# Performance work log

Measured on AMD Instinct MI355X. Metric: run time of the kernel, lower is better.

## Reference

```python
import jax, jax.numpy as jnp
import numpy as np

B, T, D = 32, 256, 512
P, V = 2048, 40000
DFF = 2148
K_CONCEPT = 50
K_PHENO = 10
EPS = 1e-6


def setup_inputs() -> dict:
    key = jax.random.key(0)
    ks = jax.random.split(key, 10)
    return {
        "visit_embeddings": jax.random.normal(ks[0], (B, T, D), jnp.float32) * 0.05,
        "visit_mask": jax.random.randint(ks[1], (B, T), 0, 2, jnp.int32),
        "embedding_matrix": jax.random.normal(ks[2], (V, D), jnp.float32) * 0.05,
        "phenotype_embeddings": jax.random.normal(ks[3], (P, D), jnp.float32) * 0.05,
        "w1": jax.random.normal(ks[4], (D, DFF), jnp.float32) * (1.0 / np.sqrt(D)),
        "b1": jnp.zeros((DFF,), jnp.float32),
        "w2": jax.random.normal(ks[5], (DFF, D), jnp.float32) * (1.0 / np.sqrt(DFF)),
        "b2": jnp.zeros((D,), jnp.float32),
        "ln1_g": jnp.ones((D,), jnp.float32),
        "ln1_b": jnp.zeros((D,), jnp.float32),
        "ln2_g": jnp.ones((D,), jnp.float32),
        "ln2_b": jnp.zeros((D,), jnp.float32),
    }


def _layer_norm(x, g, b):
    mu = jnp.mean(x, axis=-1, keepdims=True)
    var = jnp.mean(jnp.square(x - mu), axis=-1, keepdims=True)
    return (x - mu) * jax.lax.rsqrt(var + EPS) * g + b


def _smallest_k(x, k):
    # top_k of -x selects the k smallest values per row
    return -jax.lax.top_k(-x, k)[0]


def reference(visit_embeddings, visit_mask, embedding_matrix, phenotype_embeddings,
              w1, b1, w2, b2, ln1_g, ln1_b, ln2_g, ln2_b):
    # mask: original mask==1 means padded; converted mask is 1.0 for valid positions
    conv_mask = (1.0 - visit_mask.astype(jnp.float32))[:, :, None]  # [B,T,1]

    # phenotype attention: softmax over (logits * mask)  (faithful to TF code)
    logits = jnp.einsum('btd,pd->btp', visit_embeddings, phenotype_embeddings) * conv_mask
    probs = jax.nn.softmax(logits, axis=-1)  # [B,T,P]

    # phenotype-concept euclidean distance metric (cdist + row-wise smallest-k)
    r_p = jnp.sum(phenotype_embeddings * phenotype_embeddings, axis=1)[:, None]  # [P,1]
    r_c = jnp.sum(embedding_matrix * embedding_matrix, axis=1)[None, :]          # [1,V]
    d_pc = jnp.sqrt(r_p + r_c - 2.0 * phenotype_embeddings @ embedding_matrix.T)  # [P,V]
    phenotype_concept_dist = jnp.mean(_smallest_k(d_pc, K_CONCEPT))

    # phenotype probability entropy metric
    entropy = -jnp.sum(probs * jnp.log(probs) * conv_mask, axis=-1)  # [B,T]

    # phenotype-phenotype squared-distance metrics
    d_pp = r_p - 2.0 * phenotype_embeddings @ phenotype_embeddings.T + r_p.T  # [P,P]
    near = _smallest_k(d_pp, K_PHENO)  # [P,K_PHENO]
    phe_inv_loss = jnp.mean(jnp.exp(-near))
    phe_dist_metric = jnp.mean(near)
    phe_dist_var = jnp.var(near)

    # residual + FFN block (dropout is identity at inference)
    ctx = probs @ phenotype_embeddings  # [B,T,D]
    out1 = _layer_norm(visit_embeddings + ctx, ln1_g, ln1_b)
    ffn = jnp.maximum(out1 @ w1 + b1, 0.0) @ w2 + b2
    out2 = _layer_norm(out1 + ffn, ln2_g, ln2_b)

    return (out2, probs, phenotype_concept_dist, entropy,
            phe_inv_loss, phe_dist_metric, phe_dist_var)
```

## Files before the change

kernel.cpp:

```cpp
#include <hip/hip_runtime.h>
#include <stdint.h>
#include <stddef.h>

#define BATCH 32
#define TLEN 256
#define DIM 512
#define PHE 2048
#define VOC 40000
#define VOCP 40960
#define DFF 2148
#define DFFP2 2304
#define BT 8192
#define KC 50
#define KP 10
#define CHUNK 8192
#define NCHUNK 5
#define LNEPS 1e-6f
#define BIGF 1e30f

typedef unsigned short u16;
typedef __attribute__((ext_vector_type(8))) short short8;
typedef __attribute__((ext_vector_type(8))) unsigned short ushort8;
typedef __attribute__((ext_vector_type(4))) float floatx4;

__device__ inline u16 f2bf(float f) {
  union { float f; unsigned int u; } v; v.f = f;
  unsigned int u = v.u;
  return (u16)((u + 0x7fffu + ((u >> 16) & 1u)) >> 16);
}
__device__ inline float bf2f(u16 u) {
  union { unsigned int u; float f; } c; c.u = ((unsigned int)u) << 16;
  return c.f;
}

__device__ inline unsigned int f2mono(float f) {
  union { float f; unsigned int u; } c; c.f = f;
  return (c.u & 0x80000000u) ? ~c.u : (c.u | 0x80000000u);
}
__device__ inline float mono2f(unsigned int u) {
  union { unsigned int u; float f; } c;
  c.u = (u & 0x80000000u) ? (u & 0x7FFFFFFFu) : ~u;
  return c.f;
}
__device__ inline unsigned int mono16(u16 u) {
  return (u & 0x8000u) ? (u16)~u : (u16)(u | 0x8000u);
}
__device__ inline float mono2f16(unsigned int k) {
  unsigned int ub = (k & 0x8000u) ? (k & 0x7FFFu) : ((~k) & 0xFFFFu);
  union { unsigned int u; float f; } c; c.u = ub << 16;
  return c.f;
}

__device__ inline void load_lds16(const void* g, void* l) {
  __builtin_amdgcn_global_load_lds(
      (const __attribute__((address_space(1))) unsigned int*)g,
      (__attribute__((address_space(3))) unsigned int*)l, 16, 0, 0);
}

__device__ inline float waveRedSum(float v) {
  #pragma unroll
  for (int off = 32; off > 0; off >>= 1) v += __shfl_down(v, off);
  return v;
}
__device__ inline float waveRedMax(float v) {
  #pragma unroll
  for (int off = 32; off > 0; off >>= 1) v = fmaxf(v, __shfl_down(v, off));
  return v;
}
__device__ inline float blockRedSum(float v) {
  __shared__ float sm[8];
  int lane = threadIdx.x & 63, w = threadIdx.x >> 6, nw = blockDim.x >> 6;
  v = waveRedSum(v);
  __syncthreads();
  if (lane == 0) sm[w] = v;
  __syncthreads();
  float r = 0.f;
  for (int i = 0; i < nw; ++i) r += sm[i];
  return r;
}
__device__ inline float blockRedMax(float v) {
  __shared__ float sm2[8];
  int lane = threadIdx.x & 63, w = threadIdx.x >> 6, nw = blockDim.x >> 6;
  v = waveRedMax(v);
  __syncthreads();
  if (lane == 0) sm2[w] = v;
  __syncthreads();
  float r = -BIGF;
  for (int i = 0; i < nw; ++i) r = fmaxf(r, sm2[i]);
  return r;
}
__device__ inline double blockRedSumD(double v) {
  __shared__ double red[256];
  int tid = threadIdx.x;
  __syncthreads();
  red[tid] = v;
  __syncthreads();
  for (int s = 128; s > 0; s >>= 1) {
    if (tid < s) red[tid] += red[tid + s];
    __syncthreads();
  }
  return red[0];
}

__device__ inline void hist_add2(int* hist, int digit, bool pred) {
  int lane = threadIdx.x & 63;
  unsigned long long act = __ballot(pred);
  if (!act) return;
  int src = __ffsll((long long)act) - 1;
  int ld = __shfl(digit, src);
  unsigned long long m = __ballot(pred && digit == ld);
  if (__popcll(m) >= 32) {
    if (lane == src) atomicAdd(&hist[ld], (int)__popcll(m));
    if ((act & ~m) & (1ull << lane)) atomicAdd(&hist[digit], 1);
  } else {
    if (pred) atomicAdd(&hist[digit], 1);
  }
}

__global__ void k_sentinel(float* out) { out[0] = -12345.0f; }

#define PREP_VIS 2048
#define PREP_PHT (DIM * PHE / 256)
#define PREP_W1  (DFFP2 * DIM / 256)
#define PREP_W2  (DIM * DFFP2 / 256)
__global__ void __launch_bounds__(256) k_prep(
    const float* __restrict__ emb, u16* __restrict__ emb_bf, float* __restrict__ r_c,
    const float* __restrict__ phe, u16* __restrict__ phe_bf, float* __restrict__ r_p,
    const float* __restrict__ visit, u16* __restrict__ visit_bf,
    u16* __restrict__ pheT_bf,
    const float* __restrict__ w1, u16* __restrict__ w1T_bf,
    const float* __restrict__ w2, u16* __restrict__ w2T_bf)
{
  int bid = (int)blockIdx.x, tid = threadIdx.x;
  if (bid < VOC + PHE) {
    const float* src = (bid < VOC) ? emb + (size_t)bid * DIM
                                   : phe + (size_t)(bid - VOC) * DIM;
    u16* dst = (bid < VOC) ? emb_bf + (size_t)bid * DIM
                           : phe_bf + (size_t)(bid - VOC) * DIM;
    float a = src[tid], b = src[tid + 256];
    dst[tid] = f2bf(a); dst[tid + 256] = f2bf(b);
    float s = blockRedSum(a * a + b * b);
    if (tid == 0) {
      if (bid < VOC) r_c[bid] = s; else r_p[bid - VOC] = s;
    }
    return;
  }
  int b2 = bid - (VOC + PHE);
  if (b2 < PREP_VIS) {
    int base = b2 * 2048 + tid;
    #pragma unroll
    for (int e = 0; e < 8; ++e) {
      int i = base + e * 256;
      visit_bf[i] = f2bf(visit[i]);
    }
    return;
  }
  b2 -= PREP_VIS;
  if (b2 < PREP_PHT) {
    int i = b2 * 256 + tid;
    int r = i / PHE, c = i % PHE;
    pheT_bf[i] = f2bf(phe[(size_t)c * DIM + r]);
    return;
  }
  b2 -= PREP_PHT;
  if (b2 < PREP_W1) {
    int i = b2 * 256 + tid;
    int r = i / DIM, c = i % DIM;
    float v = (r < DFF) ? w1[(size_t)c * DFF + r] : 0.f;
    w1T_bf[i] = f2bf(v);
    return;
  }
  b2 -= PREP_W1;
  {
    int i = b2 * 256 + tid;
    int r = i / DFFP2, c = i % DFFP2;
    float v = (c < DFF) ? w2[(size_t)c * DIM + r] : 0.f;
    w2T_bf[i] = f2bf(v);
    return;
  }
}

#define EPI_STORE 0
#define EPI_DPP   1
#define EPI_FFN1  3
#define EPI_FFN2  4

__device__ inline void xcd_block(int BM, int BN, int& m0, int& n0) {
  int nwg = gridDim.x * gridDim.y;
  int orig = blockIdx.y * gridDim.x + blockIdx.x;
  int q = nwg >> 3, r = nwg & 7;
  int xcd = orig & 7, i0 = orig >> 3;
  int wgid = (xcd < r ? xcd * (q + 1) : r * (q + 1) + (xcd - r) * q) + i0;
  m0 = (wgid / gridDim.x) * BM;
  n0 = (wgid % gridDim.x) * BN;
}

template<int EPI>
__device__ inline void epi_write(int rr, int col, float c,
    float* outF, u16* outU, int ldc, const float* rp,
    const float* bias, int nepi) {
  if (EPI == EPI_STORE) {
    outF[(size_t)rr * ldc + col] = c;
  } else if (EPI == EPI_DPP) {
    outF[(size_t)rr * ldc + col] = rp[rr] + rp[col] - 2.f * c;
  } else if (EPI == EPI_FFN1) {
    float h = (col < nepi) ? fmaxf(c + bias[col], 0.f) : 0.f;
    outU[(size_t)rr * ldc + col] = f2bf(h);
  } else if (EPI == EPI_FFN2) {
    outF[(size_t)rr * ldc + col] = c + bias[col];
  }
}

__device__ __forceinline__ void dpc_select(
    char* smem, int si, const u16* __restrict__ dr, int schunk,
    float* __restrict__ top)
{
  int row = si >> 1, half = si & 1;
  const u16* src = dr + (size_t)row * CHUNK + half * 4096;
  int* hist = (int*)smem;
  int* cum  = hist + 1024;
  int* wred = cum + 256;
  int* selb = wred + 8;
  int tid = threadIdx.x, lane = tid & 63, w4 = tid >> 6;
  int hbase = w4 << 8;

  unsigned int kv[16];
  #pragma unroll
  for (int j2 = 0; j2 < 2; ++j2) {
    ushort8 qv = *(const ushort8*)(src + j2 * 2048 + tid * 8);
    #pragma unroll
    for (int e = 0; e < 8; ++e) kv[j2 * 8 + e] = mono16((u16)qv[e]);
  }

  int hbmin = 255, hbmax = 0;
  #pragma unroll
  for (int j = 0; j < 16; ++j) {
    int hb = (int)(kv[j] >> 8);
    hbmin = min(hbmin, hb); hbmax = max(hbmax, hb);
  }
  #pragma unroll
  for (int off = 32; off > 0; off >>= 1) {
    hbmin = min(hbmin, __shfl_down(hbmin, off));
    hbmax = max(hbmax, __shfl_down(hbmax, off));
  }
  if (lane == 0) { wred[w4] = hbmin; wred[4 + w4] = hbmax; }
  __syncthreads();
  int bmin = min(min(wred[0], wred[1]), min(wred[2], wred[3]));
  int bmax = max(max(wred[4], wred[5]), max(wred[6], wred[7]));
  __syncthreads();

  unsigned int prefix;
  int kk = KC;
  if (bmin == bmax) {
    prefix = (unsigned int)bmin;
  } else {
    hist[tid] = 0; hist[tid + 256] = 0; hist[tid + 512] = 0; hist[tid + 768] = 0;
    __syncthreads();
    #pragma unroll
    for (int j = 0; j < 16; ++j) hist_add2(hist + hbase, (int)(kv[j] >> 8), true);
    __syncthreads();
    int x = hist[tid] + hist[tid + 256] + hist[tid + 512] + hist[tid + 768];
    #pragma unroll
    for (int off = 1; off < 64; off <<= 1) { int y = __shfl_up(x, off); if (lane >= off) x += y; }
    if (lane == 63) wred[w4] = x;
    __syncthreads();
    #pragma unroll
    for (int i = 0; i < 4; ++i) if (i < w4) x += wred[i];
    cum[tid] = x;
    __syncthreads();
    int prev = (tid == 0) ? 0 : cum[tid - 1];
    if (prev < kk && kk <= cum[tid]) { selb[0] = tid; selb[1] = kk - prev; }
    __syncthreads();
    prefix = (unsigned int)selb[0];
    kk = selb[1];
    __syncthreads();
  }

  hist[tid] = 0; hist[tid + 256] = 0; hist[tid + 512] = 0; hist[tid + 768] = 0;
  __syncthreads();
  #pragma unroll
  for (int j = 0; j < 16; ++j)
    hist_add2(hist + hbase, (int)(kv[j] & 255u), (kv[j] >> 8) == prefix);
  __syncthreads();
  int x = hist[tid] + hist[tid + 256] + hist[tid + 512] + hist[tid + 768];
  #pragma unroll
  for (int off = 1; off < 64; off <<= 1) { int y = __shfl_up(x, off); if (lane >= off) x += y; }
  if (lane == 63) wred[w4] = x;
  __syncthreads();
  #pragma unroll
  for (int i = 0; i < 4; ++i) if (i < w4) x += wred[i];
  cum[tid] = x;
  __syncthreads();
  int prev = (tid == 0) ? 0 : cum[tid - 1];
  if (prev < kk && kk <= cum[tid]) { selb[0] = tid; selb[1] = kk - prev; }
  __syncthreads();
  unsigned int key = (prefix << 8) | (unsigned int)selb[0];
  float thr = mono2f16(key);
  float* o50 = top + (size_t)row * (NCHUNK * 2 * KC) + (schunk * 2 + half) * KC;
  __syncthreads();

  int cless = 0;
  #pragma unroll
  for (int j = 0; j < 16; ++j) if (kv[j] < key) cless++;
  int xc = cless;
  #pragma unroll
  for (int off = 1; off < 64; off <<= 1) { int y = __shfl_up(xc, off); if (lane >= off) xc += y; }
  if (lane == 63) wred[w4] = xc;
  __syncthreads();
  #pragma unroll
  for (int i = 0; i < 4; ++i) if (i < w4) xc += wred[i];
  int o = xc - cless;
  #pragma unroll
  for (int j = 0; j < 16; ++j)
    if (kv[j] < key) o50[o++] = mono2f16(kv[j]);
  cum[tid] = xc;
  __syncthreads();
  int total_less = cum[255];
  for (int i = total_less + tid; i < KC; i += 256) o50[i] = thr;
}

__global__ void __launch_bounds__(256, 2) k_dpc(
    const u16* __restrict__ phe_bf, const u16* __restrict__ emb_bf,
    int gchunk, int ngemm, u16* __restrict__ dw,
    const u16* __restrict__ dr, int schunk, float* __restrict__ top,
    const float* __restrict__ rp, const float* __restrict__ rc)
{
  __shared__ __align__(16) char smem[32768];
  int bid = (int)blockIdx.x;
  if (bid < ngemm) {
    u16* As = (u16*)smem;
    u16* Bs = (u16*)(smem + 16384);
    int tid = threadIdx.x, lane = tid & 63, w = tid >> 6;
    int wm = w >> 1, wn = w & 1;
    int nwg = ngemm, orig = bid;
    int q = nwg >> 3, r = nwg & 7;
    int xcd = orig & 7, i0 = orig >> 3;
    int wgid = (xcd < r ? xcd * (q + 1) : r * (q + 1) + (xcd - r) * q) + i0;
    int m0 = (wgid >> 6) << 7;
    int n0 = (wgid & 63) << 7;
    const u16* Bm = emb_bf + (size_t)gchunk * CHUNK * DIM;
    const float* rcc = rc + gchunk * CHUNK;
    int bvalid = VOC - gchunk * CHUNK; if (bvalid > CHUNK) bvalid = CHUNK;

    floatx4 acc[4][4];
    #pragma unroll
    for (int i = 0; i < 4; ++i)
      #pragma unroll
      for (int j = 0; j < 4; ++j)
        acc[i][j] = (floatx4){0.f, 0.f, 0.f, 0.f};

    int hi = lane >> 4, rsw = lane & 7;
    for (int kt = 0; kt < DIM / 64; ++kt) {
      int k0 = kt * 64;
      #pragma unroll
      for (int p = 0; p < 4; ++p) {
        int c = p * 256 + tid;
        int row = c >> 3;
        int src16 = (c & 7) ^ (row & 7);
        load_lds16(phe_bf + (size_t)(m0 + row) * DIM + k0 + src16 * 8,
                   &As[p * 2048 + w * 512]);
      }
      #pragma unroll
      for (int p = 0; p < 4; ++p) {
        int c = p * 256 + tid;
        int row = c >> 3;
        int src16 = (c & 7) ^ (row & 7);
        load_lds16(Bm + (size_t)(n0 + row) * DIM + k0 + src16 * 8,
                   &Bs[p * 2048 + w * 512]);
      }
      __syncthreads();
      #pragma unroll
      for (int ks = 0; ks < 2; ++ks) {
        int chk = ((ks << 2) | hi) ^ rsw;
        short8 a[4], b[4];
        #pragma unroll
        for (int i = 0; i < 4; ++i)
          a[i] = *(const short8*)&As[(wm * 64 + i * 16 + (lane & 15)) * 64 + chk * 8];
        #pragma unroll
        for (int j = 0; j < 4; ++j)
          b[j] = *(const short8*)&Bs[(wn * 64 + j * 16 + (lane & 15)) * 64 + chk * 8];
        #pragma unroll
        for (int i = 0; i < 4; ++i)
          #pragma unroll
          for (int j = 0; j < 4; ++j)
            acc[i][j] = __builtin_amdgcn_mfma_f32_16x16x32_bf16(a[i], b[j], acc[i][j], 0, 0, 0);
      }
      __syncthreads();
    }
    #pragma unroll
    for (int i = 0; i < 4; ++i) {
      #pragma unroll
      for (int j = 0; j < 4; ++j) {
        floatx4 v = acc[i][j];
        int col = n0 + wn * 64 + j * 16 + (lane & 15);
        int rb = m0 + wm * 64 + i * 16 + ((lane >> 4) << 2);
        #pragma unroll
        for (int qq = 0; qq < 4; ++qq) {
          int rr = rb + qq;
          float d = (col < bvalid) ? sqrtf(fmaxf(rp[rr] + rcc[col] - 2.f * v[qq], 0.f)) : BIGF;
          dw[(size_t)rr * CHUNK + col] = f2bf(d);
        }
      }
    }
  } else {
    if (schunk < 0) return;
    dpc_select(smem, bid - ngemm, dr, schunk, top);
  }
}

__global__ void __launch_bounds__(256, 2) k_dpc_log(
    const u16* __restrict__ visit_bf, const u16* __restrict__ phe_bf,
    int ngemm, u16* __restrict__ logit_bf,
    const u16* __restrict__ dr, int schunk, float* __restrict__ top)
{
  __shared__ __align__(16) char smem[32768];
  int bid = (int)blockIdx.x;
  if (bid < ngemm) {
    u16* As = (u16*)smem;
    u16* Bs = (u16*)(smem + 16384);
    int tid = threadIdx.x, lane = tid & 63, w = tid >> 6;
    int wm = w >> 1, wn = w & 1;
    int nwg = ngemm, orig = bid;
    int q = nwg >> 3, r = nwg & 7;
    int xcd = orig & 7, i0 = orig >> 3;
    int wgid = (xcd < r ? xcd * (q + 1) : r * (q + 1) + (xcd - r) * q) + i0;
    int m0 = (wgid >> 4) << 7;
    int n0 = (wgid & 15) << 7;

    floatx4 acc[4][4];
    #pragma unroll
    for (int i = 0; i < 4; ++i)
      #pragma unroll
      for (int j = 0; j < 4; ++j)
        acc[i][j] = (floatx4){0.f, 0.f, 0.f, 0.f};

    int hi = lane >> 4, rsw = lane & 7;
    for (int kt = 0; kt < DIM / 64; ++kt) {
      int k0 = kt * 64;
      #pragma unroll
      for (int p = 0; p < 4; ++p) {
        int c = p * 256 + tid;
        int row = c >> 3;
        int src16 = (c & 7) ^ (row & 7);
        load_lds16(visit_bf + (size_t)(m0 + row) * DIM + k0 + src16 * 8,
                   &As[p * 2048 + w * 512]);
      }
      #pragma unroll
      for (int p = 0; p < 4; ++p) {
        int c = p * 256 + tid;
        int row = c >> 3;
        int src16 = (c & 7) ^ (row & 7);
        load_lds16(phe_bf + (size_t)(n0 + row) * DIM + k0 + src16 * 8,
                   &Bs[p * 2048 + w * 512]);
      }
      __syncthreads();
      #pragma unroll
      for (int ks = 0; ks < 2; ++ks) {
        int chk = ((ks << 2) | hi) ^ rsw;
        short8 a[4], b[4];
        #pragma unroll
        for (int i = 0; i < 4; ++i)
          a[i] = *(const short8*)&As[(wm * 64 + i * 16 + (lane & 15)) * 64 + chk * 8];
        #pragma unroll
        for (int j = 0; j < 4; ++j)
          b[j] = *(const short8*)&Bs[(wn * 64 + j * 16 + (lane & 15)) * 64 + chk * 8];
        #pragma unroll
        for (int i = 0; i < 4; ++i)
          #pragma unroll
          for (int j = 0; j < 4; ++j)
            acc[i][j] = __builtin_amdgcn_mfma_f32_16x16x32_bf16(a[i], b[j], acc[i][j], 0, 0, 0);
      }
      __syncthreads();
    }
    #pragma unroll
    for (int i = 0; i < 4; ++i) {
      #pragma unroll
      for (int j = 0; j < 4; ++j) {
        floatx4 v = acc[i][j];
        int col = n0 + wn * 64 + j * 16 + (lane & 15);
        int rb = m0 + wm * 64 + i * 16 + ((lane >> 4) << 2);
        #pragma unroll
        for (int qq = 0; qq < 4; ++qq)
          logit_bf[(size_t)(rb + qq) * PHE + col] = f2bf(v[qq]);
      }
    }
  } else {
    if (schunk < 0) return;
    dpc_select(smem, bid - ngemm, dr, schunk, top);
  }
}

template<int EPI, int BM, int BN, int NTH, int WR, int WC>
__global__ void __launch_bounds__(NTH, 2) k_gemm2(
    const u16* __restrict__ A, int lda,
    const u16* __restrict__ Bm, int ldb, int K,
    float* __restrict__ outF, u16* __restrict__ outU, int ldc,
    const float* __restrict__ rp, const float* __restrict__ bias, int nepi)
{
  constexpr int BK = 64;
  constexpr int MR = BM / WR / 16;
  constexpr int NR = BN / WC / 16;
  constexpr int LD_A = BM * BK / (NTH * 8);
  constexpr int LD_B = BN * BK / (NTH * 8);
  __shared__ __align__(16) u16 As[2][BM * BK];
  __shared__ __align__(16) u16 Bs[2][BN * BK];
  int tid = threadIdx.x, lane = tid & 63, w = tid >> 6;
  int wm = w / WC, wn = w % WC;
  int m0, n0;
  xcd_block(BM, BN, m0, n0);

  floatx4 acc[MR][NR];
  #pragma unroll
  for (int i = 0; i < MR; ++i)
    #pragma unroll
    for (int j = 0; j < NR; ++j)
      acc[i][j] = (floatx4){0.f, 0.f, 0.f, 0.f};

  auto stage = [&](int buf, int k0) {
    #pragma unroll
    for (int p = 0; p < LD_A; ++p) {
      int c = p * NTH + tid;
      int row = c >> 3;
      int src16 = (c & 7) ^ (row & 7);
      load_lds16(A + (size_t)(m0 + row) * lda + k0 + src16 * 8,
                 &As[buf][p * NTH * 8 + w * 512]);
    }
    #pragma unroll
    for (int p = 0; p < LD_B; ++p) {
      int c = p * NTH + tid;
      int row = c >> 3;
      int src16 = (c & 7) ^ (row & 7);
      load_lds16(Bm + (size_t)(n0 + row) * ldb + k0 + src16 * 8,
                 &Bs[buf][p * NTH * 8 + w * 512]);
    }
  };

  int nt = K / BK;
  stage(0, 0);
  __syncthreads();
  int cur = 0;
  int hi = lane >> 4;
  int rsw = lane & 7;
  for (int kt = 0; kt < nt; ++kt) {
    if (kt + 1 < nt) stage(cur ^ 1, (kt + 1) * BK);
    #pragma unroll
    for (int ks = 0; ks < 2; ++ks) {
      int chk = ((ks << 2) | hi) ^ rsw;
      short8 a[MR], b[NR];
      #pragma unroll
      for (int i = 0; i < MR; ++i)
        a[i] = *(const short8*)&As[cur][(wm * (BM / WR) + i * 16 + (lane & 15)) * BK + chk * 8];
      #pragma unroll
      for (int j = 0; j < NR; ++j)
        b[j] = *(const short8*)&Bs[cur][(wn * (BN / WC) + j * 16 + (lane & 15)) * BK + chk * 8];
      #pragma unroll
      for (int i = 0; i < MR; ++i)
        #pragma unroll
        for (int j = 0; j < NR; ++j)
          acc[i][j] = __builtin_amdgcn_mfma_f32_16x16x32_bf16(a[i], b[j], acc[i][j], 0, 0, 0);
    }
    __syncthreads();
    cur ^= 1;
  }

  #pragma unroll
  for (int i = 0; i < MR; ++i) {
    #pragma unroll
    for (int j = 0; j < NR; ++j) {
      floatx4 v = acc[i][j];
      int col = n0 + wn * (BN / WC) + j * 16 + (lane & 15);
      int rb = m0 + wm * (BM / WR) + i * 16 + ((lane >> 4) << 2);
      #pragma unroll
      for (int qq = 0; qq < 4; ++qq)
        epi_write<EPI>(rb + qq, col, v[qq], outF, outU, ldc, rp, bias, nepi);
    }
  }
}

template<int EPI>
__global__ void __launch_bounds__(256, 4) k_gemm2s(
    const u16* __restrict__ A, int lda,
    const u16* __restrict__ Bm, int ldb, int K,
    float* __restrict__ outF, u16* __restrict__ outU, int ldc,
    const float* __restrict__ rp, const float* __restrict__ bias, int nepi)
{
  constexpr int BM = 128, BN = 128, BK = 64, NTH = 256;
  constexpr int MR = 4, NR = 4;
  __shared__ __align__(16) u16 As[BM * BK];
  __shared__ __align__(16) u16 Bs[BN * BK];
  int tid = threadIdx.x, lane = tid & 63, w = tid >> 6;
  int wm = w >> 1, wn = w & 1;
  int m0, n0;
  xcd_block(BM, BN, m0, n0);

  floatx4 acc[MR][NR];
  #pragma unroll
  for (int i = 0; i < MR; ++i)
    #pragma unroll
    for (int j = 0; j < NR; ++j)
      acc[i][j] = (floatx4){0.f, 0.f, 0.f, 0.f};

  int hi = lane >> 4;
  int rsw = lane & 7;
  int nt = K / BK;
  for (int kt = 0; kt < nt; ++kt) {
    int k0 = kt * BK;
    #pragma unroll
    for (int p = 0; p < 4; ++p) {
      int c = p * NTH + tid;
      int row = c >> 3;
      int src16 = (c & 7) ^ (row & 7);
      load_lds16(A + (size_t)(m0 + row) * lda + k0 + src16 * 8,
                 &As[p * NTH * 8 + w * 512]);
    }
    #pragma unroll
    for (int p = 0; p < 4; ++p) {
      int c = p * NTH + tid;
      int row = c >> 3;
      int src16 = (c & 7) ^ (row & 7);
      load_lds16(Bm + (size_t)(n0 + row) * ldb + k0 + src16 * 8,
                 &Bs[p * NTH * 8 + w * 512]);
    }
    __syncthreads();
    #pragma unroll
    for (int ks = 0; ks < 2; ++ks) {
      int chk = ((ks << 2) | hi) ^ rsw;
      short8 a[MR], b[NR];
      #pragma unroll
      for (int i = 0; i < MR; ++i)
        a[i] = *(const short8*)&As[(wm * 64 + i * 16 + (lane & 15)) * BK + chk * 8];
      #pragma unroll
      for (int j = 0; j < NR; ++j)
        b[j] = *(const short8*)&Bs[(wn * 64 + j * 16 + (lane & 15)) * BK + chk * 8];
      #pragma unroll
      for (int i = 0; i < MR; ++i)
        #pragma unroll
        for (int j = 0; j < NR; ++j)
          acc[i][j] = __builtin_amdgcn_mfma_f32_16x16x32_bf16(a[i], b[j], acc[i][j], 0, 0, 0);
    }
    __syncthreads();
  }

  #pragma unroll
  for (int i = 0; i < MR; ++i) {
    #pragma unroll
    for (int j = 0; j < NR; ++j) {
      floatx4 v = acc[i][j];
      int col = n0 + wn * 64 + j * 16 + (lane & 15);
      int rb = m0 + wm * 64 + i * 16 + ((lane >> 4) << 2);
      #pragma unroll
      for (int qq = 0; qq < 4; ++qq)
        epi_write<EPI>(rb + qq, col, v[qq], outF, outU, ldc, rp, bias, nepi);
    }
  }
}

__global__ void __launch_bounds__(256) k_softmax(
    u16* __restrict__ probs_bf, const int* __restrict__ mask,
    float* __restrict__ probs, float* __restrict__ entropy)
{
  int row = blockIdx.x;
  int tid = threadIdx.x;
  u16* pb = probs_bf + (size_t)row * PHE;
  float* pp = probs + (size_t)row * PHE;
  if (mask[row] != 0) {
    const float u = 1.0f / (float)PHE;
    const u16 ub = f2bf(u);
    for (int i = tid; i < PHE; i += 256) { pp[i] = u; pb[i] = ub; }
    if (tid == 0) entropy[row] = 0.f;
    return;
  }
  float l[8];
  float mx = -BIGF;
  #pragma unroll
  for (int j = 0; j < 8; ++j) { l[j] = bf2f(pb[tid + j * 256]); mx = fmaxf(mx, l[j]); }
  mx = blockRedMax(mx);
  float s = 0.f;
  #pragma unroll
  for (int j = 0; j < 8; ++j) { l[j] = __expf(l[j] - mx); s += l[j]; }
  s = blockRedSum(s);
  float inv = 1.0f / s;
  float ent = 0.f;
  #pragma unroll
  for (int j = 0; j < 8; ++j) {
    float p = l[j] * inv;
    pp[tid + j * 256] = p;
    pb[tid + j * 256] = f2bf(p);
    ent += p * __logf(p);
  }
  ent = blockRedSum(ent);
  if (tid == 0) entropy[row] = -ent;
}

__global__ void __launch_bounds__(256) k_ln(
    const float* __restrict__ xa, const float* __restrict__ xb,
    const float* __restrict__ g, const float* __restrict__ bb,
    float* __restrict__ outF, u16* __restrict__ outBf)
{
  int row = blockIdx.x;
  int tid = threadIdx.x;
  const float* pa = xa + (size_t)row * DIM;
  const float* pb = xb + (size_t)row * DIM;
  float x0 = pa[tid] + pb[tid];
  float x1 = pa[tid + 256] + pb[tid + 256];
  float mu = blockRedSum(x0 + x1) * (1.0f / DIM);
  float d0 = x0 - mu, d1 = x1 - mu;
  float var = blockRedSum(d0 * d0 + d1 * d1) * (1.0f / DIM);
  float rs = 1.0f / sqrtf(var + LNEPS);
  float y0 = d0 * rs * g[tid] + bb[tid];
  float y1 = d1 * rs * g[tid + 256] + bb[tid + 256];
  if (outF) {
    outF[(size_t)row * DIM + tid] = y0;
    outF[(size_t)row * DIM + tid + 256] = y1;
  }
  if (outBf) {
    outBf[(size_t)row * DIM + tid] = f2bf(y0);
    outBf[(size_t)row * DIM + tid + 256] = f2bf(y1);
  }
}

template<int NPER>
__global__ void __launch_bounds__(256) k_rsel(
    const float* __restrict__ in, int ldin, int ncols, int k, int mode,
    float* __restrict__ out)
{
  __shared__ int hist[1024];
  __shared__ int cum[256];
  __shared__ int wsum[4];
  __shared__ int sel_bucket, sel_rank;
  int row = blockIdx.x;
  int tid = threadIdx.x;
  int lane = tid & 63, w = tid >> 6;
  int hbase = w << 8;
  const float* src = in + (size_t)row * ldin;

  unsigned int v[NPER];
  #pragma unroll
  for (int j = 0; j < NPER; ++j) {
    int idx = tid + j * 256;
    v[j] = (idx < ncols) ? f2mono(src[idx]) : 0xFFFFFFFFu;
  }

  unsigned int prefix = 0, pmask = 0;
  int kk = k;
  for (int shift = 24; shift >= 0; shift -= 8) {
    hist[tid] = 0; hist[tid + 256] = 0; hist[tid + 512] = 0; hist[tid + 768] = 0;
    __syncthreads();
    #pragma unroll
    for (int j = 0; j < NPER; ++j)
      hist_add2(hist + hbase, (int)((v[j] >> shift) & 255), (v[j] & pmask) == prefix);
    __syncthreads();
    int x = hist[tid] + hist[tid + 256] + hist[tid + 512] + hist[tid + 768];
    #pragma unroll
    for (int off = 1; off < 64; off <<= 1) {
      int y = __shfl_up(x, off);
      if (lane >= off) x += y;
    }
    if (lane == 63) wsum[w] = x;
    __syncthreads();
    #pragma unroll
    for (int i = 0; i < 4; ++i) if (i < w) x += wsum[i];
    cum[tid] = x;
    __syncthreads();
    int prev = (tid == 0) ? 0 : cum[tid - 1];
    if (prev < kk && kk <= cum[tid]) { sel_bucket = tid; sel_rank = kk - prev; }
    __syncthreads();
    prefix |= ((unsigned int)sel_bucket) << shift;
    pmask |= 255u << shift;
    kk = sel_rank;
    __syncthreads();
  }

  float thr = mono2f(prefix);
  int need = kk;

  float s = 0.f, se = 0.f, sq = 0.f;
  #pragma unroll
  for (int j = 0; j < NPER; ++j) {
    if (v[j] < prefix) {
      float f = mono2f(v[j]);
      s += f; se += __expf(-f); sq += f * f;
    }
  }
  float ts = blockRedSum(s);
  float tse = blockRedSum(se);
  float tsq = blockRedSum(sq);
  if (tid == 0) {
    float fn = (float)need;
    ts += fn * thr;
    if (mode == 1) {
      out[row] = ts;
    } else {
      tse += fn * __expf(-thr);
      tsq += fn * thr * thr;
      out[(size_t)row * 4] = ts;
      out[(size_t)row * 4 + 1] = tse;
      out[(size_t)row * 4 + 2] = tsq;
    }
  }
}

__global__ void __launch_bounds__(256) k_final(
    const float* __restrict__ row_sum50, const float* __restrict__ pp_part,
    float* __restrict__ out_pcd, float* __restrict__ out_inv,
    float* __restrict__ out_mean, float* __restrict__ out_var)
{
  int tid = threadIdx.x;
  double s50 = 0, sn = 0, se = 0, sq = 0;
  for (int i = tid; i < PHE; i += 256) {
    s50 += (double)row_sum50[i];
    sn += (double)pp_part[(size_t)i * 4];
    se += (double)pp_part[(size_t)i * 4 + 1];
    sq += (double)pp_part[(size_t)i * 4 + 2];
  }
  s50 = blockRedSumD(s50);
  sn = blockRedSumD(sn);
  se = blockRedSumD(se);
  sq = blockRedSumD(sq);
  if (tid == 0) {
    *out_pcd = (float)(s50 / (double)(PHE * KC));
    double mean = sn / (double)(PHE * KP);
    *out_inv = (float)(se / (double)(PHE * KP));
    *out_mean = (float)mean;
    *out_var = (float)(sq / (double)(PHE * KP) - mean * mean);
  }
}

extern "C" void kernel_launch(void* const* d_in, const int* in_sizes, int n_in,
                              void* d_out, int out_size, void* d_ws, size_t ws_size,
                              hipStream_t stream)
{
  const float* visit = (const float*)d_in[0];
  const int*   vmask = (const int*)d_in[1];
  const float* emb   = (const float*)d_in[2];
  const float* phe   = (const float*)d_in[3];
  const float* w1    = (const float*)d_in[4];
  const float* b1    = (const float*)d_in[5];
  const float* w2    = (const float*)d_in[6];
  const float* b2    = (const float*)d_in[7];
  const float* ln1g  = (const float*)d_in[8];
  const float* ln1b  = (const float*)d_in[9];
  const float* ln2g  = (const float*)d_in[10];
  const float* ln2b  = (const float*)d_in[11];

  float* out = (float*)d_out;
  float* out2      = out;
  float* probs     = out + (size_t)BT * DIM;
  float* pcd       = probs + (size_t)BT * PHE;
  float* entropy   = pcd + 1;
  float* inv_loss  = entropy + BT;
  float* dist_mean = inv_loss + 1;
  float* dist_var  = dist_mean + 1;

  char* wsb = (char*)d_ws;
  size_t off = 0;
  auto alloc = [&](size_t bytes) -> char* {
    char* p = wsb + off;
    off = (off + bytes + 255) & ~(size_t)255;
    return p;
  };
  u16* phe_bf   = (u16*)alloc((size_t)PHE * DIM * 2);
  u16* pheT_bf  = (u16*)alloc((size_t)DIM * PHE * 2);
  u16* visit_bf = (u16*)alloc((size_t)BT * DIM * 2);
  u16* w1T_bf   = (u16*)alloc((size_t)DFFP2 * DIM * 2);
  u16* w2T_bf   = (u16*)alloc((size_t)DIM * DFFP2 * 2);
  float* r_p    = (float*)alloc((size_t)PHE * 4);
  float* r_c    = (float*)alloc((size_t)VOC * 4);
  char* big1    = alloc((size_t)67108864);
  char* big2    = alloc((size_t)VOCP * DIM * 2);
  float* top50c = (float*)alloc((size_t)PHE * NCHUNK * 2 * KC * 4);
  char* big3    = alloc((size_t)PHE * PHE * 4);
  u16* probs_bf = (u16*)alloc((size_t)BT * PHE * 2);
  float* out1_f = (float*)alloc((size_t)BT * DIM * 4);
  u16* out1_bf  = (u16*)alloc((size_t)BT * DIM * 2);
  float* ffn_f  = (float*)alloc((size_t)BT * DIM * 4);
  float* row_sum50 = (float*)alloc((size_t)PHE * 4);
  float* pp_part   = (float*)alloc((size_t)PHE * 4 * 4);

  u16* dchunk0  = (u16*)big1;
  u16* dchunk1  = (u16*)(big1 + 33554432);
  u16* emb_bf   = (u16*)big2;
  u16* h_bf     = (u16*)big2;
  float* d_pp   = (float*)big3;
  float* ctx_f  = (float*)big3;

  if (ws_size < off) { k_sentinel<<<1, 1, 0, stream>>>(out); return; }

  int nprep = (VOC + PHE) + PREP_VIS + PREP_PHT + PREP_W1 + PREP_W2;
  k_prep<<<nprep, 256, 0, stream>>>(emb, emb_bf, r_c, phe, phe_bf, r_p,
                                    visit, visit_bf, pheT_bf, w1, w1T_bf, w2, w2T_bf);

  for (int c = 0; c < NCHUNK; ++c) {
    int s = c - 1;
    int nsel = (s >= 0) ? PHE * 2 : 0;
    u16* dw = (c & 1) ? dchunk1 : dchunk0;
    u16* dr = (s >= 0) ? ((s & 1) ? dchunk1 : dchunk0) : nullptr;
    k_dpc<<<1024 + nsel, 256, 0, stream>>>(
        phe_bf, emb_bf, c, 1024, dw, dr, s, top50c, r_p, r_c);
  }
  k_dpc_log<<<1024 + PHE * 2, 256, 0, stream>>>(
      visit_bf, phe_bf, 1024, probs_bf,
      (NCHUNK - 1) & 1 ? dchunk1 : dchunk0, NCHUNK - 1, top50c);
  k_rsel<2><<<PHE, 256, 0, stream>>>(top50c, NCHUNK * 2 * KC, NCHUNK * 2 * KC, KC, 1, row_sum50);

  k_gemm2<EPI_DPP, 128, 128, 256, 2, 2><<<dim3(PHE / 128, PHE / 128), 256, 0, stream>>>(
      phe_bf, DIM, phe_bf, DIM, DIM, d_pp, nullptr, PHE, r_p, nullptr, 0);
  k_rsel<8><<<PHE, 256, 0, stream>>>(d_pp, PHE, PHE, KP, 2, pp_part);

  k_softmax<<<BT, 256, 0, stream>>>(probs_bf, vmask, probs, entropy);
  k_gemm2<EPI_STORE, 64, 128, 256, 2, 2><<<dim3(DIM / 128, BT / 64), 256, 0, stream>>>(
      probs_bf, PHE, pheT_bf, PHE, PHE, ctx_f, nullptr, DIM, nullptr, nullptr, 0);

  k_ln<<<BT, 256, 0, stream>>>(visit, ctx_f, ln1g, ln1b, out1_f, out1_bf);
  k_gemm2s<EPI_FFN1><<<dim3(DFFP2 / 128, BT / 128), 256, 0, stream>>>(
      out1_bf, DIM, w1T_bf, DIM, DIM, nullptr, h_bf, DFFP2, nullptr, b1, DFF);
  k_gemm2<EPI_FFN2, 64, 128, 256, 2, 2><<<dim3(DIM / 128, BT / 64), 256, 0, stream>>>(
      h_bf, DFFP2, w2T_bf, DFFP2, DFFP2, ffn_f, nullptr, DIM, nullptr, b2, 0);
  k_ln<<<BT, 256, 0, stream>>>(out1_f, ffn_f, ln2g, ln2b, out2, nullptr);

  k_final<<<1, 256, 0, stream>>>(row_sum50, pp_part, pcd, inv_loss, dist_mean, dist_var);
}
```

Measured before the change: 575.6 us.

## Spread bf16 preparation work across dpc chunk launches to overlap with GEMM

The monolithic prep kernel is split. Only the phenotype rows and the first embedding chunk are converted up front. Conversion of each later embedding chunk, plus the visit, pheT, w1T and w2T conversions, is appended as extra blocks to the chunked d_pc GEMM/select launches, so this memory-bound work runs alongside compute-bound GEMM tiles and the standalone prep is shorter. The risk is that the extra blocks compete for CUs with the GEMM and select blocks. Correctness also depends on chunk c+1 being converted before the launch that reads it, which stream ordering guarantees.

```diff
diff --git a/kernel.cpp b/kernel.cpp
--- a/kernel.cpp
+++ b/kernel.cpp
@@ -119,65 +119,22 @@
 
 __global__ void k_sentinel(float* out) { out[0] = -12345.0f; }
 
-#define PREP_VIS 2048
-#define PREP_PHT (DIM * PHE / 256)
-#define PREP_W1  (DFFP2 * DIM / 256)
-#define PREP_W2  (DIM * DFFP2 / 256)
-__global__ void __launch_bounds__(256) k_prep(
-    const float* __restrict__ emb, u16* __restrict__ emb_bf, float* __restrict__ r_c,
+__global__ void __launch_bounds__(256) k_prep_a(
     const float* __restrict__ phe, u16* __restrict__ phe_bf, float* __restrict__ r_p,
-    const float* __restrict__ visit, u16* __restrict__ visit_bf,
-    u16* __restrict__ pheT_bf,
-    const float* __restrict__ w1, u16* __restrict__ w1T_bf,
-    const float* __restrict__ w2, u16* __restrict__ w2T_bf)
+    const float* __restrict__ emb, u16* __restrict__ emb_bf, float* __restrict__ r_c)
 {
   int bid = (int)blockIdx.x, tid = threadIdx.x;
-  if (bid < VOC + PHE) {
-    const float* src = (bid < VOC) ? emb + (size_t)bid * DIM
-                                   : phe + (size_t)(bid - VOC) * DIM;
-    u16* dst = (bid < VOC) ? emb_bf + (size_t)bid * DIM
-                           : phe_bf + (size_t)(bid - VOC) * DIM;
-    float a = src[tid], b = src[tid + 256];
-    dst[tid] = f2bf(a); dst[tid + 256] = f2bf(b);
-    float s = blockRedSum(a * a + b * b);
-    if (tid == 0) {
-      if (bid < VOC) r_c[bid] = s; else r_p[bid - VOC] = s;
-    }
-    return;
-  }
-  int b2 = bid - (VOC + PHE);
-  if (b2 < PREP_VIS) {
-    int base = b2 * 2048 + tid;
-    #pragma unroll
-    for (int e = 0; e < 8; ++e) {
-      int i = base + e * 256;
-      visit_bf[i] = f2bf(visit[i]);
-    }
-    return;
-  }
-  b2 -= PREP_VIS;
-  if (b2 < PREP_PHT) {
-    int i = b2 * 256 + tid;
-    int r = i / PHE, c = i % PHE;
-    pheT_bf[i] = f2bf(phe[(size_t)c * DIM + r]);
-    return;
-  }
-  b2 -= PREP_PHT;
-  if (b2 < PREP_W1) {
-    int i = b2 * 256 + tid;
-    int r = i / DIM, c = i % DIM;
-    float v = (r < DFF) ? w1[(size_t)c * DFF + r] : 0.f;
-    w1T_bf[i] = f2bf(v);
-    return;
-  }
-  b2 -= PREP_W1;
-  {
-    int i = b2 * 256 + tid;
-    int r = i / DFFP2, c = i % DFFP2;
-    float v = (c < DFF) ? w2[(size_t)c * DIM + r] : 0.f;
-    w2T_bf[i] = f2bf(v);
-    return;
-  }
+  const float* src; u16* dst; float* rout;
+  if (bid < PHE) {
+    src = phe + (size_t)bid * DIM; dst = phe_bf + (size_t)bid * DIM; rout = r_p + bid;
+  } else {
+    int row = bid - PHE;
+    src = emb + (size_t)row * DIM; dst = emb_bf + (size_t)row * DIM; rout = r_c + row;
+  }
+  float a = src[tid], b = src[tid + 256];
+  dst[tid] = f2bf(a); dst[tid + 256] = f2bf(b);
+  float s = blockRedSum(a * a + b * b);
+  if (tid == 0) *rout = s;
 }
 
 #define EPI_STORE 0
@@ -320,17 +277,24 @@
 }
 
 __global__ void __launch_bounds__(256, 2) k_dpc(
-    const u16* __restrict__ phe_bf, const u16* __restrict__ emb_bf,
+    const u16* __restrict__ phe_bf, const u16* emb_bf,
     int gchunk, int ngemm, u16* __restrict__ dw,
     const u16* __restrict__ dr, int schunk, float* __restrict__ top,
-    const float* __restrict__ rp, const float* __restrict__ rc)
+    const float* __restrict__ rp, const float* __restrict__ rc, int nsel,
+    int ncvt, int cvtbase, const float* __restrict__ embf, u16* emb_bf_w,
+    float* __restrict__ r_c_w,
+    int nvis, const float* __restrict__ visitf, u16* __restrict__ visit_bf,
+    int npht, const float* __restrict__ phef, u16* __restrict__ pheT_bf,
+    int nw1, const float* __restrict__ w1, u16* __restrict__ w1T_bf,
+    int nw2, const float* __restrict__ w2, u16* __restrict__ w2T_bf)
 {
   __shared__ __align__(16) char smem[32768];
   int bid = (int)blockIdx.x;
+  int tid = threadIdx.x;
   if (bid < ngemm) {
     u16* As = (u16*)smem;
     u16* Bs = (u16*)(smem + 16384);
-    int tid = threadIdx.x, lane = tid & 63, w = tid >> 6;
+    int lane = tid & 63, w = tid >> 6;
     int wm = w >> 1, wn = w & 1;
     int nwg = ngemm, orig = bid;
     int q = nwg >> 3, r = nwg & 7;
@@ -402,9 +366,59 @@
         }
       }
     }
-  } else {
-    if (schunk < 0) return;
-    dpc_select(smem, bid - ngemm, dr, schunk, top);
+    return;
+  }
+  bid -= ngemm;
+  if (bid < nsel) {
+    if (schunk >= 0) dpc_select(smem, bid, dr, schunk, top);
+    return;
+  }
+  bid -= nsel;
+  if (bid < ncvt) {
+    int row = cvtbase + bid;
+    const float* src = embf + (size_t)row * DIM;
+    u16* dst = emb_bf_w + (size_t)row * DIM;
+    float a = src[tid], b = src[tid + 256];
+    dst[tid] = f2bf(a); dst[tid + 256] = f2bf(b);
+    float s = waveRedSum(a * a + b * b);
+    float* red = (float*)smem;
+    if ((tid & 63) == 0) red[tid >> 6] = s;
+    __syncthreads();
+    if (tid == 0) r_c_w[row] = red[0] + red[1] + red[2] + red[3];
+    return;
+  }
+  bid -= ncvt;
+  if (bid < nvis) {
+    int base = bid * 2048 + tid;
+    #pragma unroll
+    for (int e = 0; e < 8; ++e) {
+      int i = base + e * 256;
+      visit_bf[i] = f2bf(visitf[i]);
+    }
+    return;
+  }
+  bid -= nvis;
+  if (bid < npht) {
+    int i = bid * 256 + tid;
+    int r = i >> 11, c = i & 2047;
+    pheT_bf[i] = f2bf(phef[(size_t)c * DIM + r]);
+    return;
+  }
+  bid -= npht;
+  if (bid < nw1) {
+    int i = bid * 256 + tid;
+    int r = i >> 9, c = i & 511;
+    float v = (r < DFF) ? w1[(size_t)c * DFF + r] : 0.f;
+    w1T_bf[i] = f2bf(v);
+    return;
+  }
+  bid -= nw1;
+  if (bid < nw2) {
+    int i = bid * 256 + tid;
+    int r = i / DFFP2, c = i % DFFP2;
+    float v = (c < DFF) ? w2[(size_t)c * DIM + r] : 0.f;
+    w2T_bf[i] = f2bf(v);
+    return;
   }
 }
 
@@ -886,17 +900,26 @@
 
   if (ws_size < off) { k_sentinel<<<1, 1, 0, stream>>>(out); return; }
 
-  int nprep = (VOC + PHE) + PREP_VIS + PREP_PHT + PREP_W1 + PREP_W2;
-  k_prep<<<nprep, 256, 0, stream>>>(emb, emb_bf, r_c, phe, phe_bf, r_p,
-                                    visit, visit_bf, pheT_bf, w1, w1T_bf, w2, w2T_bf);
+  k_prep_a<<<PHE + CHUNK, 256, 0, stream>>>(phe, phe_bf, r_p, emb, emb_bf, r_c);
 
   for (int c = 0; c < NCHUNK; ++c) {
     int s = c - 1;
     int nsel = (s >= 0) ? PHE * 2 : 0;
+    int cvtc = c + 1;
+    int ncvt = (cvtc < NCHUNK) ? ((VOC - cvtc * CHUNK < CHUNK) ? VOC - cvtc * CHUNK : CHUNK) : 0;
+    int nvis = (c == 0) ? 2048 : 0;
+    int npht = (c == 0) ? (DIM * PHE / 256) : 0;
+    int nw1  = (c == 0) ? (DFFP2 * DIM / 256) : 0;
+    int nw2  = (c == 0) ? (DIM * DFFP2 / 256) : 0;
     u16* dw = (c & 1) ? dchunk1 : dchunk0;
-    u16* dr = (s >= 0) ? ((s & 1) ? dchunk1 : dchunk0) : nullptr;
-    k_dpc<<<1024 + nsel, 256, 0, stream>>>(
-        phe_bf, emb_bf, c, 1024, dw, dr, s, top50c, r_p, r_c);
+    const u16* dr = (s >= 0) ? ((s & 1) ? dchunk1 : dchunk0) : nullptr;
+    k_dpc<<<1024 + nsel + ncvt + nvis + npht + nw1 + nw2, 256, 0, stream>>>(
+        phe_bf, emb_bf, c, 1024, dw, dr, s, top50c, r_p, r_c, nsel,
+        ncvt, cvtc * CHUNK, emb, emb_bf, r_c,
+        nvis, visit, visit_bf,
+        npht, phe, pheT_bf,
+        nw1, w1, w1T_bf,
+        nw2, w2, w2T_bf);
   }
   k_dpc_log<<<1024 + PHE * 2, 256, 0, stream>>>(
       visit_bf, phe_bf, 1024, probs_bf,
```

New measurement: 592.3 us. 2.9% more time.
